# Kernel optimization log

Measured on AMD Instinct MI355X. Metric: run time of the kernel, lower is better.

The kernel has to match this reference:

```python
import jax, jax.numpy as jnp
import numpy as np

N, E = 20000, 320000
FX, FW, FH, H = 256, 128, 128, 4  # x feat, walk feat, hidden=end_embd, heads


def _gat(x, edge_index, W, a_s, a_d, R):
    # W: [H,Fin,Fout]; a_s,a_d: [H,Fout]; R: [Fin,Fout] residual projection
    n = x.shape[0]
    h = jnp.einsum('nf,hfo->hno', x, W)                      # [H,N,Fout]
    src, dst = edge_index[0], edge_index[1]
    s_src = jnp.einsum('hno,ho->nh', h, a_s)                 # [N,H]
    s_dst = jnp.einsum('hno,ho->nh', h, a_d)                 # [N,H]
    e = jax.nn.leaky_relu(s_src[src] + s_dst[dst], 0.2)      # [E,H] per-edge scores
    m = jax.ops.segment_max(e, src, num_segments=n)          # scatter-softmax (stable)
    ex = jnp.exp(e - m[src])
    den = jax.ops.segment_sum(ex, src, num_segments=n)
    alpha = ex / (den[src] + 1e-16)                          # [E,H]
    msg = jnp.transpose(h, (1, 0, 2))[dst] * alpha[:, :, None]        # [E,H,Fout]
    agg = jax.ops.segment_sum(msg, src, num_segments=n).mean(axis=1)  # [N,Fout]
    return jax.nn.elu(agg + x @ R)


def _forward(x, dat, W1, a1s, a1d, R1, W2, a2s, a2d, R2,
             Wd1, ad1s, ad1d, Rd1, Wd2, ad2s, ad2d, Rd2,
             fc1_w, fc1_b, fc2_w, fc2_b, conv_w, conv_b, edge_index):
    x1 = _gat(x, edge_index, W1, a1s, a1d, R1)
    x2 = _gat(x1, edge_index, W2, a2s, a2d, R2)
    d1 = _gat(dat, edge_index, Wd1, ad1s, ad1d, Rd1)
    d2 = _gat(d1, edge_index, Wd2, ad2s, ad2d, Rd2)
    n = x.shape[0]
    # cat on feature dim, transpose, view(1, l*2, end_size, N)
    xd = jnp.concatenate([x1, x2, d1, d2], axis=1).T.reshape(1, 4, FH, n)
    avg = xd.mean(axis=(2, 3))                               # SE global avg pool [1,4]
    att = jax.nn.sigmoid((avg @ fc1_w + fc1_b) @ fc2_w + fc2_b)  # no act between fc1/fc2 (as in source)
    xatt = jax.nn.relu(att[:, :, None, None] * xd)
    y = jnp.einsum('bchn,c->bhn', xatt, conv_w) + conv_b     # 1x1 conv, 4->1 channels
    return y.reshape(FH, n).T                                # dropout = identity (eval)


def setup_inputs():
    key = jax.random.key(0)
    ks = jax.random.split(key, 26)

    def rn(k, shape, s=0.1):
        return jax.random.normal(k, shape, jnp.float32) * s

    return {
        'x': jax.random.normal(ks[0], (N, FX), jnp.float32),
        'dat': jax.random.normal(ks[1], (N, FW), jnp.float32),
        'W1': rn(ks[2], (H, FX, FH)), 'a1s': rn(ks[3], (H, FH)), 'a1d': rn(ks[4], (H, FH)), 'R1': rn(ks[5], (FX, FH)),
        'W2': rn(ks[6], (H, FH, FH)), 'a2s': rn(ks[7], (H, FH)), 'a2d': rn(ks[8], (H, FH)), 'R2': rn(ks[9], (FH, FH)),
        'Wd1': rn(ks[10], (H, FW, FH)), 'ad1s': rn(ks[11], (H, FH)), 'ad1d': rn(ks[12], (H, FH)), 'Rd1': rn(ks[13], (FW, FH)),
        'Wd2': rn(ks[14], (H, FH, FH)), 'ad2s': rn(ks[15], (H, FH)), 'ad2d': rn(ks[16], (H, FH)), 'Rd2': rn(ks[17], (FH, FH)),
        'fc1_w': rn(ks[18], (4, 20)), 'fc1_b': jnp.zeros((20,), jnp.float32),
        'fc2_w': rn(ks[19], (20, 4)), 'fc2_b': jnp.zeros((4,), jnp.float32),
        'conv_w': rn(ks[20], (4,)), 'conv_b': jnp.zeros((), jnp.float32),
        'edge_index': jax.random.randint(ks[21], (2, E), 0, N, dtype=jnp.int32),
    }


def reference(x, dat, W1, a1s, a1d, R1, W2, a2s, a2d, R2,
              Wd1, ad1s, ad1d, Rd1, Wd2, ad2s, ad2d, Rd2,
              fc1_w, fc1_b, fc2_w, fc2_b, conv_w, conv_b, edge_index):
    return _forward(x, dat, W1, a1s, a1d, R1, W2, a2s, a2d, R2,
                    Wd1, ad1s, ad1d, Rd1, Wd2, ad2s, ad2d, Rd2,
                    fc1_w, fc1_b, fc2_w, fc2_b, conv_w, conv_b, edge_index)
```

## Files before the change

### kernel.cpp

```cpp
#include <hip/hip_runtime.h>
#include <hip/hip_bf16.h>
#include <math.h>

#define NN 20000
#define EE 320000
#define FXX 256
#define FWW 128
#define NH 4

typedef __attribute__((ext_vector_type(8))) short short8v;
typedef __attribute__((ext_vector_type(4))) float f32x4;

static __device__ __forceinline__ float bf2f(unsigned short s) {
    unsigned int u = ((unsigned int)s) << 16;
    return __builtin_bit_cast(float, u);
}

static __device__ __forceinline__ unsigned short f2bf_u16(float f) {
    unsigned int u = __builtin_bit_cast(unsigned int, f);
    unsigned int r = 0x7fffu + ((u >> 16) & 1u);
    return (unsigned short)((u + r) >> 16);
}

struct WscItem { const float* W; const float* as_; const float* ad_; int Fin; };
struct WscParams { WscItem t[4]; };

__global__ __launch_bounds__(256) void wsc_kernel(WscParams p, float* __restrict__ wsc)
{
    int L = blockIdx.z;
    WscItem it = p.t[L];
    int wid = threadIdx.x >> 6, lane = threadIdx.x & 63;
    int r = blockIdx.x * 4 + wid;
    if (r >= it.Fin * 4) return;
    int h = r / it.Fin, k = r - h * it.Fin;
    float2 w2 = *(const float2*)(it.W + ((size_t)(h * it.Fin + k)) * 128 + 2 * lane);
    float2 s2 = *(const float2*)(it.as_ + h * 128 + 2 * lane);
    float2 d2 = *(const float2*)(it.ad_ + h * 128 + 2 * lane);
    float vs = w2.x * s2.x + w2.y * s2.y;
    float vd = w2.x * d2.x + w2.y * d2.y;
    #pragma unroll
    for (int o = 32; o; o >>= 1) { vs += __shfl_xor(vs, o); vd += __shfl_xor(vd, o); }
    if (lane == 0) {
        wsc[(size_t)L * 2048 + h * 256 + k] = vs;
        wsc[(size_t)L * 2048 + (4 + h) * 256 + k] = vd;
    }
}

struct WcItem { const float* W; const float* R; __hip_bfloat16* dst; int Fin; int KK; int total; };
struct WcParams { WcItem t[4]; };

__global__ __launch_bounds__(256) void wcomb_kernel(WcParams p)
{
    WcItem it = p.t[blockIdx.z];
    int idx = blockIdx.x * 256 + threadIdx.x;
    if (idx >= it.total) return;
    int c = idx / it.KK;
    int k5 = idx - c * it.KK;
    int f4 = it.Fin * 4;
    float v;
    if (k5 < f4) {
        int h = k5 / it.Fin, k = k5 - h * it.Fin;
        v = 0.25f * it.W[((size_t)(h * it.Fin + k)) * 128 + c];
    } else {
        v = it.R[(size_t)(k5 - f4) * 128 + c];
    }
    it.dst[(size_t)c * it.KK + k5] = __float2bfloat16(v);
}

template<int CF>
static __device__ __forceinline__ void cast_score_body(const float* __restrict__ Xf,
                                                       __hip_bfloat16* __restrict__ Xb,
                                                       const float* __restrict__ wsc,
                                                       float* __restrict__ ssrc,
                                                       float* __restrict__ sdst)
{
    const int Fin = CF * 64;
    int wid = threadIdx.x >> 6, lane = threadIdx.x & 63;
    int n = blockIdx.x * 4 + wid;
    if (n >= NN) return;
    int c0 = lane * CF;
    float xv[CF];
    #pragma unroll
    for (int i = 0; i < CF; ++i) xv[i] = Xf[(size_t)n * Fin + c0 + i];
    union { unsigned u[CF / 2]; unsigned short s[CF]; } pk;
    #pragma unroll
    for (int i = 0; i < CF; ++i) pk.s[i] = f2bf_u16(xv[i]);
    #pragma unroll
    for (int w = 0; w < CF / 2; ++w)
        *(unsigned*)(Xb + (size_t)n * Fin + c0 + w * 2) = pk.u[w];
    float acc[8];
    #pragma unroll
    for (int j = 0; j < 8; ++j) {
        const float* w = wsc + j * 256 + c0;
        float s = 0.f;
        #pragma unroll
        for (int i = 0; i < CF; ++i) s += xv[i] * w[i];
        acc[j] = s;
    }
    #pragma unroll
    for (int o = 32; o; o >>= 1)
        #pragma unroll
        for (int j = 0; j < 8; ++j) acc[j] += __shfl_xor(acc[j], o);
    if (lane == 0) {
        *(float4*)(ssrc + (size_t)n * 4) = make_float4(acc[0], acc[1], acc[2], acc[3]);
        *(float4*)(sdst + (size_t)n * 4) = make_float4(acc[4], acc[5], acc[6], acc[7]);
    }
}

struct CSPair {
    const float* Xf[2]; __hip_bfloat16* Xb[2];
    const float* wsc[2]; float* ssrc[2]; float* sdst[2];
};

__global__ __launch_bounds__(256) void cast_score_pair(CSPair p)
{
    if (blockIdx.y == 0)
        cast_score_body<4>(p.Xf[0], p.Xb[0], p.wsc[0], p.ssrc[0], p.sdst[0]);
    else
        cast_score_body<2>(p.Xf[1], p.Xb[1], p.wsc[1], p.ssrc[1], p.sdst[1]);
}

__global__ __launch_bounds__(256) void hist_kernel(const int* __restrict__ src, int* __restrict__ cnt)
{
    int i = blockIdx.x * blockDim.x + threadIdx.x;
    if (i < EE) atomicAdd(&cnt[src[i]], 1);
}

__global__ __launch_bounds__(1024) void scan_kernel(const int* __restrict__ cnt, int* __restrict__ row_ptr)
{
    __shared__ int lds[1024];
    int t = threadIdx.x;
    const int CH = 20;
    int start = t * CH, end = start + CH; if (end > NN) end = NN;
    int sum = 0;
    if (start < NN) for (int i = start; i < end; ++i) sum += cnt[i];
    lds[t] = sum;
    __syncthreads();
    for (int o = 1; o < 1024; o <<= 1) {
        int v = (t >= o) ? lds[t - o] : 0;
        __syncthreads();
        lds[t] += v;
        __syncthreads();
    }
    int run = lds[t] - sum;
    if (start < NN) for (int i = start; i < end; ++i) { row_ptr[i] = run; run += cnt[i]; }
    if (t == 1023) row_ptr[NN] = lds[1023];
}

__global__ __launch_bounds__(256) void scatter_kernel(const int* __restrict__ src,
                                                      const int* __restrict__ dst,
                                                      const int* __restrict__ row_ptr,
                                                      int* __restrict__ off,
                                                      int* __restrict__ csr_dst)
{
    int i = blockIdx.x * blockDim.x + threadIdx.x;
    if (i >= EE) return;
    int s = src[i];
    int p = row_ptr[s] + atomicAdd(&off[s], 1);
    csr_dst[p] = dst[i];
}

template<int CF>
static __device__ __forceinline__ void agg_body(const __hip_bfloat16* __restrict__ Xb,
                                                const float* __restrict__ ssrc,
                                                const float* __restrict__ sdst,
                                                const int* __restrict__ row_ptr,
                                                const int* __restrict__ csr_dst,
                                                __hip_bfloat16* __restrict__ Cat)
{
    const int Fin = CF * 64, F4 = 4 * Fin;
    int wid = threadIdx.x >> 6, lane = threadIdx.x & 63;
    int n = blockIdx.x * 4 + wid;
    if (n >= NN) return;
    int r0 = row_ptr[n], r1 = row_ptr[n + 1];
    int deg = r1 - r0;

    float acc[4][CF] = {};

    if (deg > 0) {
        float4 sn = *(const float4*)(ssrc + (size_t)n * 4);
        auto comp_e = [&](int s, int& dout) -> float4 {
            int d = csr_dst[r0 + s];
            dout = d;
            float4 sd = *(const float4*)(sdst + (size_t)d * 4);
            float4 e; float v;
            v = sn.x + sd.x; e.x = v >= 0.f ? v : 0.2f * v;
            v = sn.y + sd.y; e.y = v >= 0.f ? v : 0.2f * v;
            v = sn.z + sd.z; e.z = v >= 0.f ? v : 0.2f * v;
            v = sn.w + sd.w; e.w = v >= 0.f ? v : 0.2f * v;
            return e;
        };

        float4 e0 = make_float4(-1e30f, -1e30f, -1e30f, -1e30f);
        int d0 = 0;
        if (lane < deg) e0 = comp_e(lane, d0);
        float4 m = e0;
        for (int s = lane + 64; s < deg; s += 64) {
            int dt; float4 ev = comp_e(s, dt);
            m.x = fmaxf(m.x, ev.x); m.y = fmaxf(m.y, ev.y);
            m.z = fmaxf(m.z, ev.z); m.w = fmaxf(m.w, ev.w);
        }
        #pragma unroll
        for (int o = 32; o; o >>= 1) {
            m.x = fmaxf(m.x, __shfl_xor(m.x, o));
            m.y = fmaxf(m.y, __shfl_xor(m.y, o));
            m.z = fmaxf(m.z, __shfl_xor(m.z, o));
            m.w = fmaxf(m.w, __shfl_xor(m.w, o));
        }
        float4 p0 = make_float4(0.f, 0.f, 0.f, 0.f);
        if (lane < deg) {
            p0.x = expf(e0.x - m.x); p0.y = expf(e0.y - m.y);
            p0.z = expf(e0.z - m.z); p0.w = expf(e0.w - m.w);
        }
        float4 den = p0;
        for (int s = lane + 64; s < deg; s += 64) {
            int dt; float4 ev = comp_e(s, dt);
            den.x += expf(ev.x - m.x); den.y += expf(ev.y - m.y);
            den.z += expf(ev.z - m.z); den.w += expf(ev.w - m.w);
        }
        #pragma unroll
        for (int o = 32; o; o >>= 1) {
            den.x += __shfl_xor(den.x, o); den.y += __shfl_xor(den.y, o);
            den.z += __shfl_xor(den.z, o); den.w += __shfl_xor(den.w, o);
        }
        den.x = 1.f / (den.x + 1e-16f); den.y = 1.f / (den.y + 1e-16f);
        den.z = 1.f / (den.z + 1e-16f); den.w = 1.f / (den.w + 1e-16f);

        float4 a0;
        a0.x = p0.x * den.x; a0.y = p0.y * den.y;
        a0.z = p0.z * den.z; a0.w = p0.w * den.w;

        int cnt0 = min(deg, 64);
        int last = cnt0 - 1;
        for (int base = 0; base < cnt0; base += 4) {
            int j1 = min(base + 1, last), j2 = min(base + 2, last), j3 = min(base + 3, last);
            int dv0 = __shfl(d0, base), dv1 = __shfl(d0, j1);
            int dv2 = __shfl(d0, j2),   dv3 = __shfl(d0, j3);
            union U { unsigned u[CF / 2]; unsigned short s[CF]; };
            U l0, l1, l2, l3;
            #pragma unroll
            for (int w = 0; w < CF / 2; ++w)
                l0.u[w] = *(const unsigned*)(Xb + (size_t)dv0 * Fin + lane * CF + w * 2);
            #pragma unroll
            for (int w = 0; w < CF / 2; ++w)
                l1.u[w] = *(const unsigned*)(Xb + (size_t)dv1 * Fin + lane * CF + w * 2);
            #pragma unroll
            for (int w = 0; w < CF / 2; ++w)
                l2.u[w] = *(const unsigned*)(Xb + (size_t)dv2 * Fin + lane * CF + w * 2);
            #pragma unroll
            for (int w = 0; w < CF / 2; ++w)
                l3.u[w] = *(const unsigned*)(Xb + (size_t)dv3 * Fin + lane * CF + w * 2);

            {
                float ax = __shfl(a0.x, base), ay = __shfl(a0.y, base);
                float az = __shfl(a0.z, base), aw = __shfl(a0.w, base);
                #pragma unroll
                for (int i = 0; i < CF; ++i) {
                    float xv = bf2f(l0.s[i]);
                    acc[0][i] += ax * xv; acc[1][i] += ay * xv;
                    acc[2][i] += az * xv; acc[3][i] += aw * xv;
                }
            }
            if (base + 1 < cnt0) {
                float ax = __shfl(a0.x, j1), ay = __shfl(a0.y, j1);
                float az = __shfl(a0.z, j1), aw = __shfl(a0.w, j1);
                #pragma unroll
                for (int i = 0; i < CF; ++i) {
                    float xv = bf2f(l1.s[i]);
                    acc[0][i] += ax * xv; acc[1][i] += ay * xv;
                    acc[2][i] += az * xv; acc[3][i] += aw * xv;
                }
            }
            if (base + 2 < cnt0) {
                float ax = __shfl(a0.x, j2), ay = __shfl(a0.y, j2);
                float az = __shfl(a0.z, j2), aw = __shfl(a0.w, j2);
                #pragma unroll
                for (int i = 0; i < CF; ++i) {
                    float xv = bf2f(l2.s[i]);
                    acc[0][i] += ax * xv; acc[1][i] += ay * xv;
                    acc[2][i] += az * xv; acc[3][i] += aw * xv;
                }
            }
            if (base + 3 < cnt0) {
                float ax = __shfl(a0.x, j3), ay = __shfl(a0.y, j3);
                float az = __shfl(a0.z, j3), aw = __shfl(a0.w, j3);
                #pragma unroll
                for (int i = 0; i < CF; ++i) {
                    float xv = bf2f(l3.s[i]);
                    acc[0][i] += ax * xv; acc[1][i] += ay * xv;
                    acc[2][i] += az * xv; acc[3][i] += aw * xv;
                }
            }
        }

        for (int r = r0 + 64; r < r1; r += 64) {
            int cnt = min(64, r1 - r);
            int d = 0;
            float4 a4 = make_float4(0.f, 0.f, 0.f, 0.f);
            if (r + lane < r1) {
                int dt;
                float4 ev = comp_e(r - r0 + lane, dt);
                d = dt;
                a4.x = expf(ev.x - m.x) * den.x; a4.y = expf(ev.y - m.y) * den.y;
                a4.z = expf(ev.z - m.z) * den.z; a4.w = expf(ev.w - m.w) * den.w;
            }
            for (int j = 0; j < cnt; ++j) {
                int ddv = __shfl(d, j);
                float ax = __shfl(a4.x, j), ay = __shfl(a4.y, j);
                float az = __shfl(a4.z, j), aw = __shfl(a4.w, j);
                union { unsigned u[CF / 2]; unsigned short s[CF]; } ld;
                #pragma unroll
                for (int w = 0; w < CF / 2; ++w)
                    ld.u[w] = *(const unsigned*)(Xb + (size_t)ddv * Fin + lane * CF + w * 2);
                #pragma unroll
                for (int i = 0; i < CF; ++i) {
                    float xv = bf2f(ld.s[i]);
                    acc[0][i] += ax * xv; acc[1][i] += ay * xv;
                    acc[2][i] += az * xv; acc[3][i] += aw * xv;
                }
            }
        }
    }

    __hip_bfloat16* crow = Cat + (size_t)n * F4;
    #pragma unroll
    for (int h = 0; h < 4; ++h) {
        union { unsigned u[CF / 2]; unsigned short s[CF]; } pk;
        #pragma unroll
        for (int i = 0; i < CF; ++i) pk.s[i] = f2bf_u16(acc[h][i]);
        #pragma unroll
        for (int w = 0; w < CF / 2; ++w)
            *(unsigned*)(crow + h * Fin + lane * CF + w * 2) = pk.u[w];
    }
}

struct AggPair {
    const __hip_bfloat16* Xb[2];
    const float* ssrc[2]; const float* sdst[2];
    __hip_bfloat16* Cat[2];
};

template<int CF0, int CF1>
__global__ __launch_bounds__(256) void agg_pair_kernel(AggPair p,
                                                       const int* __restrict__ row_ptr,
                                                       const int* __restrict__ csr_dst)
{
    if (blockIdx.y == 0)
        agg_body<CF0>(p.Xb[0], p.ssrc[0], p.sdst[0], row_ptr, csr_dst, p.Cat[0]);
    else
        agg_body<CF1>(p.Xb[1], p.ssrc[1], p.sdst[1], row_ptr, csr_dst, p.Cat[1]);
}

struct GemmArgs {
    const __hip_bfloat16 *Cat, *Xb, *Wct;
    float* xout; __hip_bfloat16* xbout;
    const float* wscN; float *ssrcN, *sdstN;
    int F4, FIN, ch;
};
struct GemmPair { GemmArgs g[2]; };

__global__ __launch_bounds__(256) void gemm_pair_kernel(GemmPair p, float* __restrict__ sums)
{
    GemmArgs a = (blockIdx.y == 0) ? p.g[0] : p.g[1];
    const int F4 = a.F4, FIN = a.FIN;
    const int KK = F4 + FIN;
    const int BK = 64;
    const int NIT = KK / BK;
    __shared__ short As[2][32 * 72];
    __shared__ short Bs[2][128 * 72];
    __shared__ float ls[4];
    __shared__ float sred[4][4][4][8];

    int tid = threadIdx.x, lane = tid & 63, wid = tid >> 6;
    int wr = wid >> 1, wc = wid & 1;
    int ar = lane & 15, kg = lane >> 4;
    int row0 = blockIdx.x * 32;

    int a_row = tid >> 3, a_seg = tid & 7;
    int b_col = tid >> 1, b_seg0 = (tid & 1) * 4;

    const __hip_bfloat16* AgC = a.Cat + (size_t)(row0 + a_row) * F4 + a_seg * 8;
    const __hip_bfloat16* AgX = a.Xb + (size_t)(row0 + a_row) * FIN + a_seg * 8;
    const __hip_bfloat16* Bg = a.Wct + (size_t)b_col * KK + b_seg0 * 8;

    short8v fa, fb0, fb1, fb2, fb3;
    f32x4 acc[4] = {};

    fa  = *(const short8v*)(AgC);
    fb0 = *(const short8v*)(Bg);
    fb1 = *(const short8v*)(Bg + 8);
    fb2 = *(const short8v*)(Bg + 16);
    fb3 = *(const short8v*)(Bg + 24);
    *(short8v*)(&As[0][a_row * 72 + a_seg * 8]) = fa;
    *(short8v*)(&Bs[0][b_col * 72 + (b_seg0 + 0) * 8]) = fb0;
    *(short8v*)(&Bs[0][b_col * 72 + (b_seg0 + 1) * 8]) = fb1;
    *(short8v*)(&Bs[0][b_col * 72 + (b_seg0 + 2) * 8]) = fb2;
    *(short8v*)(&Bs[0][b_col * 72 + (b_seg0 + 3) * 8]) = fb3;

    int cur = 0;
    for (int it = 0; it < NIT; ++it) {
        if (it + 1 < NIT) {
            int kb = (it + 1) * BK;
            fa  = (kb < F4) ? *(const short8v*)(AgC + kb) : *(const short8v*)(AgX + (kb - F4));
            fb0 = *(const short8v*)(Bg + kb);
            fb1 = *(const short8v*)(Bg + kb + 8);
            fb2 = *(const short8v*)(Bg + kb + 16);
            fb3 = *(const short8v*)(Bg + kb + 24);
        }
        __syncthreads();
        #pragma unroll
        for (int ks = 0; ks < 2; ++ks) {
            short8v av = *(const short8v*)(&As[cur][(wr * 16 + ar) * 72 + ks * 32 + kg * 8]);
            #pragma unroll
            for (int nb = 0; nb < 4; ++nb) {
                short8v bv = *(const short8v*)(&Bs[cur][(wc * 64 + nb * 16 + ar) * 72 + ks * 32 + kg * 8]);
                acc[nb] = __builtin_amdgcn_mfma_f32_16x16x32_bf16(av, bv, acc[nb], 0, 0, 0);
            }
        }
        if (it + 1 < NIT) {
            int nb2 = cur ^ 1;
            *(short8v*)(&As[nb2][a_row * 72 + a_seg * 8]) = fa;
            *(short8v*)(&Bs[nb2][b_col * 72 + (b_seg0 + 0) * 8]) = fb0;
            *(short8v*)(&Bs[nb2][b_col * 72 + (b_seg0 + 1) * 8]) = fb1;
            *(short8v*)(&Bs[nb2][b_col * 72 + (b_seg0 + 2) * 8]) = fb2;
            *(short8v*)(&Bs[nb2][b_col * 72 + (b_seg0 + 3) * 8]) = fb3;
        }
        cur ^= 1;
    }

    float lsum = 0.f;
    float vpost[4][4];
    int rsub = (lane >> 4) * 4;
    #pragma unroll
    for (int nb = 0; nb < 4; ++nb) {
        int col = wc * 64 + nb * 16 + ar;
        #pragma unroll
        for (int r = 0; r < 4; ++r) {
            int row = row0 + wr * 16 + rsub + r;
            float v = acc[nb][r];
            v = v > 0.f ? v : expm1f(v);
            vpost[nb][r] = v;
            lsum += v;
            a.xout[(size_t)row * 128 + col] = v;
            a.xbout[(size_t)row * 128 + col] = __float2bfloat16(v);
        }
    }
    #pragma unroll
    for (int o = 32; o; o >>= 1) lsum += __shfl_xor(lsum, o);
    if (lane == 0) ls[wid] = lsum;

    bool dosc = a.wscN != nullptr;
    if (dosc) {
        float sc[4][8] = {};
        #pragma unroll
        for (int j = 0; j < 8; ++j) {
            #pragma unroll
            for (int nb = 0; nb < 4; ++nb) {
                float wv = a.wscN[j * 256 + wc * 64 + nb * 16 + ar];
                #pragma unroll
                for (int r = 0; r < 4; ++r) sc[r][j] += vpost[nb][r] * wv;
            }
        }
        #pragma unroll
        for (int o = 8; o; o >>= 1)
            #pragma unroll
            for (int r = 0; r < 4; ++r)
                #pragma unroll
                for (int j = 0; j < 8; ++j) sc[r][j] += __shfl_xor(sc[r][j], o);
        if (ar == 0) {
            int grp = lane >> 4;
            #pragma unroll
            for (int r = 0; r < 4; ++r)
                #pragma unroll
                for (int j = 0; j < 8; ++j) sred[wid][grp][r][j] = sc[r][j];
        }
    }
    __syncthreads();
    if (tid == 0) atomicAdd(&sums[a.ch], ls[0] + ls[1] + ls[2] + ls[3]);
    if (dosc) {
        int row_local = tid >> 3, j = tid & 7;
        int w_r = row_local >> 4, grp = (row_local >> 2) & 3, r = row_local & 3;
        float total = sred[w_r * 2 + 0][grp][r][j] + sred[w_r * 2 + 1][grp][r][j];
        int row = row0 + row_local;
        if (j < 4) a.ssrcN[(size_t)row * 4 + j] = total;
        else       a.sdstN[(size_t)row * 4 + (j - 4)] = total;
    }
}

__global__ void att_kernel(const float* __restrict__ sums,
                           const float* __restrict__ fc1w, const float* __restrict__ fc1b,
                           const float* __restrict__ fc2w, const float* __restrict__ fc2b,
                           float* __restrict__ att)
{
    if (threadIdx.x != 0 || blockIdx.x != 0) return;
    float avg[4];
    for (int c = 0; c < 4; ++c) avg[c] = sums[c] * (1.f / (NN * 128.f));
    float z[20];
    for (int j = 0; j < 20; ++j) {
        float v = fc1b[j];
        for (int c = 0; c < 4; ++c) v += avg[c] * fc1w[c * 20 + j];
        z[j] = v;
    }
    for (int c = 0; c < 4; ++c) {
        float v = fc2b[c];
        for (int j = 0; j < 20; ++j) v += z[j] * fc2w[j * 4 + c];
        att[c] = 1.f / (1.f + expf(-v));
    }
}

__global__ __launch_bounds__(256) void final_kernel(const float* __restrict__ x1,
                                                    const float* __restrict__ x2,
                                                    const float* __restrict__ d1,
                                                    const float* __restrict__ d2,
                                                    const float* __restrict__ att,
                                                    const float* __restrict__ convw,
                                                    const float* __restrict__ convb,
                                                    float* __restrict__ out)
{
    int i = blockIdx.x * blockDim.x + threadIdx.x;
    if (i >= NN * 128) return;
    float a0 = att[0], a1 = att[1], a2 = att[2], a3 = att[3];
    float w0 = convw[0], w1 = convw[1], w2 = convw[2], w3 = convw[3];
    float v = convb[0];
    v += w0 * fmaxf(a0 * x1[i], 0.f);
    v += w1 * fmaxf(a1 * x2[i], 0.f);
    v += w2 * fmaxf(a2 * d1[i], 0.f);
    v += w3 * fmaxf(a3 * d2[i], 0.f);
    out[i] = v;
}

extern "C" void kernel_launch(void* const* d_in, const int* in_sizes, int n_in,
                              void* d_out, int out_size, void* d_ws, size_t ws_size,
                              hipStream_t stream)
{
    (void)in_sizes; (void)n_in; (void)out_size; (void)ws_size;
    const float* x    = (const float*)d_in[0];
    const float* dat  = (const float*)d_in[1];
    const float* W1   = (const float*)d_in[2];
    const float* a1s  = (const float*)d_in[3];
    const float* a1d  = (const float*)d_in[4];
    const float* R1   = (const float*)d_in[5];
    const float* W2   = (const float*)d_in[6];
    const float* a2s  = (const float*)d_in[7];
    const float* a2d  = (const float*)d_in[8];
    const float* R2   = (const float*)d_in[9];
    const float* Wd1  = (const float*)d_in[10];
    const float* ad1s = (const float*)d_in[11];
    const float* ad1d = (const float*)d_in[12];
    const float* Rd1  = (const float*)d_in[13];
    const float* Wd2  = (const float*)d_in[14];
    const float* ad2s = (const float*)d_in[15];
    const float* ad2d = (const float*)d_in[16];
    const float* Rd2  = (const float*)d_in[17];
    const float* fc1w = (const float*)d_in[18];
    const float* fc1b = (const float*)d_in[19];
    const float* fc2w = (const float*)d_in[20];
    const float* fc2b = (const float*)d_in[21];
    const float* convw= (const float*)d_in[22];
    const float* convb= (const float*)d_in[23];
    const int*   eidx = (const int*)d_in[24];
    const int* esrc = eidx;
    const int* edst = eidx + EE;
    float* out = (float*)d_out;

    char* base = (char*)d_ws;
    size_t woff = 0;
    auto alloc = [&](size_t bytes) -> void* {
        void* p = base + woff;
        woff = (woff + bytes + 255) & ~(size_t)255;
        return p;
    };
    __hip_bfloat16* Cat0 = (__hip_bfloat16*)alloc((size_t)NN * 1024 * 2);
    __hip_bfloat16* Cat2 = (__hip_bfloat16*)alloc((size_t)NN * 512 * 2);
    float* X1    = (float*)alloc((size_t)NN * 128 * 4);
    float* X2    = (float*)alloc((size_t)NN * 128 * 4);
    float* D1    = (float*)alloc((size_t)NN * 128 * 4);
    float* D2    = (float*)alloc((size_t)NN * 128 * 4);
    __hip_bfloat16* XbX   = (__hip_bfloat16*)alloc((size_t)NN * FXX * 2);
    __hip_bfloat16* XbDat = (__hip_bfloat16*)alloc((size_t)NN * FWW * 2);
    __hip_bfloat16* Xb1   = (__hip_bfloat16*)alloc((size_t)NN * 128 * 2);
    __hip_bfloat16* XbD1  = (__hip_bfloat16*)alloc((size_t)NN * 128 * 2);
    __hip_bfloat16* XbTmp = (__hip_bfloat16*)alloc((size_t)NN * 128 * 2);
    __hip_bfloat16* XbTm2 = (__hip_bfloat16*)alloc((size_t)NN * 128 * 2);
    float* Wsc   = (float*)alloc((size_t)4 * 2048 * 4);
    __hip_bfloat16* Wct0 = (__hip_bfloat16*)alloc((size_t)128 * 1280 * 2);
    __hip_bfloat16* Wct1 = (__hip_bfloat16*)alloc((size_t)128 * 640 * 2);
    __hip_bfloat16* Wct2 = (__hip_bfloat16*)alloc((size_t)128 * 640 * 2);
    __hip_bfloat16* Wct3 = (__hip_bfloat16*)alloc((size_t)128 * 640 * 2);
    float* SsrcX = (float*)alloc((size_t)NN * 4 * 4);
    float* SdstX = (float*)alloc((size_t)NN * 4 * 4);
    float* Ssrc1 = (float*)alloc((size_t)NN * 4 * 4);
    float* Sdst1 = (float*)alloc((size_t)NN * 4 * 4);
    float* SsrcD = (float*)alloc((size_t)NN * 4 * 4);
    float* SdstD = (float*)alloc((size_t)NN * 4 * 4);
    float* Ssrc3 = (float*)alloc((size_t)NN * 4 * 4);
    float* Sdst3 = (float*)alloc((size_t)NN * 4 * 4);
    int* RowPtr  = (int*)alloc((size_t)(NN + 1) * 4);
    int* Cnt     = (int*)alloc((size_t)NN * 4);
    int* Off     = (int*)alloc((size_t)NN * 4);
    int* CsrDst  = (int*)alloc((size_t)EE * 4);
    float* Sums  = (float*)alloc(16);
    float* Att   = (float*)alloc(16);

    {
        WscParams WP;
        WP.t[0] = { W1,  a1s,  a1d,  FXX };
        WP.t[1] = { W2,  a2s,  a2d,  FWW };
        WP.t[2] = { Wd1, ad1s, ad1d, FWW };
        WP.t[3] = { Wd2, ad2s, ad2d, FWW };
        wsc_kernel<<<dim3(256, 1, 4), 256, 0, stream>>>(WP, Wsc);
        WcParams CP;
        CP.t[0] = { W1,  R1,  Wct0, FXX, 1280, 128 * 1280 };
        CP.t[1] = { W2,  R2,  Wct1, FWW, 640,  128 * 640 };
        CP.t[2] = { Wd1, Rd1, Wct2, FWW, 640,  128 * 640 };
        CP.t[3] = { Wd2, Rd2, Wct3, FWW, 640,  128 * 640 };
        wcomb_kernel<<<dim3(640, 1, 4), 256, 0, stream>>>(CP);
        CSPair CS;
        CS.Xf[0] = x;   CS.Xb[0] = XbX;   CS.wsc[0] = Wsc;            CS.ssrc[0] = SsrcX; CS.sdst[0] = SdstX;
        CS.Xf[1] = dat; CS.Xb[1] = XbDat; CS.wsc[1] = Wsc + 2 * 2048; CS.ssrc[1] = SsrcD; CS.sdst[1] = SdstD;
        cast_score_pair<<<dim3((NN + 3) / 4, 2), 256, 0, stream>>>(CS);
    }
    hipMemsetAsync(Cnt, 0, (size_t)NN * 4, stream);
    hipMemsetAsync(Off, 0, (size_t)NN * 4, stream);
    hipMemsetAsync(Sums, 0, 16, stream);
    hist_kernel<<<(EE + 255) / 256, 256, 0, stream>>>(esrc, Cnt);
    scan_kernel<<<1, 1024, 0, stream>>>(Cnt, RowPtr);
    scatter_kernel<<<(EE + 255) / 256, 256, 0, stream>>>(esrc, edst, RowPtr, Off, CsrDst);

    {
        AggPair AP;
        AP.Xb[0] = XbX;   AP.ssrc[0] = SsrcX; AP.sdst[0] = SdstX; AP.Cat[0] = Cat0;
        AP.Xb[1] = XbDat; AP.ssrc[1] = SsrcD; AP.sdst[1] = SdstD; AP.Cat[1] = Cat2;
        agg_pair_kernel<4, 2><<<dim3((NN + 3) / 4, 2), 256, 0, stream>>>(AP, RowPtr, CsrDst);
    }
    {
        GemmPair GP;
        GP.g[0] = { Cat0, XbX,   Wct0, X1, Xb1,  Wsc + 1 * 2048, Ssrc1, Sdst1, 1024, 256, 0 };
        GP.g[1] = { Cat2, XbDat, Wct2, D1, XbD1, Wsc + 3 * 2048, Ssrc3, Sdst3, 512,  128, 2 };
        gemm_pair_kernel<<<dim3(NN / 32, 2), 256, 0, stream>>>(GP, Sums);
    }
    {
        AggPair AP;
        AP.Xb[0] = Xb1;  AP.ssrc[0] = Ssrc1; AP.sdst[0] = Sdst1; AP.Cat[0] = Cat0;
        AP.Xb[1] = XbD1; AP.ssrc[1] = Ssrc3; AP.sdst[1] = Sdst3; AP.Cat[1] = Cat2;
        agg_pair_kernel<2, 2><<<dim3((NN + 3) / 4, 2), 256, 0, stream>>>(AP, RowPtr, CsrDst);
    }
    {
        GemmPair GP;
        GP.g[0] = { Cat0, Xb1,  Wct1, X2, XbTmp, nullptr, nullptr, nullptr, 512, 128, 1 };
        GP.g[1] = { Cat2, XbD1, Wct3, D2, XbTm2, nullptr, nullptr, nullptr, 512, 128, 3 };
        gemm_pair_kernel<<<dim3(NN / 32, 2), 256, 0, stream>>>(GP, Sums);
    }

    att_kernel<<<1, 64, 0, stream>>>(Sums, fc1w, fc1b, fc2w, fc2b, Att);
    final_kernel<<<(NN * 128 + 255) / 256, 256, 0, stream>>>(X1, X2, D1, D2, Att, convw, convb, out);
}
```

Before: 307.4 us.

## Drop fp32 layer outputs, fuse SE attention into bf16 final kernel

The GEMM epilogue no longer writes fp32 copies of each layer output, and only bf16 outputs are kept. The final combine kernel reads the four bf16 tensors two elements at a time and recomputes the small SE attention MLP per thread, which removes the separate single-thread att kernel launch. This cuts global write and read traffic roughly in half for those tensors. In exchange the final output is computed from bf16-rounded activations, and every thread repeats the tiny MLP.

```diff
diff --git a/kernel.cpp b/kernel.cpp
--- a/kernel.cpp
+++ b/kernel.cpp
@@ -353,7 +353,7 @@
 
 struct GemmArgs {
     const __hip_bfloat16 *Cat, *Xb, *Wct;
-    float* xout; __hip_bfloat16* xbout;
+    __hip_bfloat16* xbout;
     const float* wscN; float *ssrcN, *sdstN;
     int F4, FIN, ch;
 };
@@ -441,7 +441,6 @@
             v = v > 0.f ? v : expm1f(v);
             vpost[nb][r] = v;
             lsum += v;
-            a.xout[(size_t)row * 128 + col] = v;
             a.xbout[(size_t)row * 128 + col] = __float2bfloat16(v);
         }
     }
@@ -487,46 +486,56 @@
     }
 }
 
-__global__ void att_kernel(const float* __restrict__ sums,
-                           const float* __restrict__ fc1w, const float* __restrict__ fc1b,
-                           const float* __restrict__ fc2w, const float* __restrict__ fc2b,
-                           float* __restrict__ att)
-{
-    if (threadIdx.x != 0 || blockIdx.x != 0) return;
-    float avg[4];
-    for (int c = 0; c < 4; ++c) avg[c] = sums[c] * (1.f / (NN * 128.f));
-    float z[20];
-    for (int j = 0; j < 20; ++j) {
-        float v = fc1b[j];
-        for (int c = 0; c < 4; ++c) v += avg[c] * fc1w[c * 20 + j];
-        z[j] = v;
-    }
-    for (int c = 0; c < 4; ++c) {
-        float v = fc2b[c];
-        for (int j = 0; j < 20; ++j) v += z[j] * fc2w[j * 4 + c];
-        att[c] = 1.f / (1.f + expf(-v));
-    }
-}
-
-__global__ __launch_bounds__(256) void final_kernel(const float* __restrict__ x1,
-                                                    const float* __restrict__ x2,
-                                                    const float* __restrict__ d1,
-                                                    const float* __restrict__ d2,
-                                                    const float* __restrict__ att,
+__global__ __launch_bounds__(256) void final_kernel(const __hip_bfloat16* __restrict__ x1,
+                                                    const __hip_bfloat16* __restrict__ x2,
+                                                    const __hip_bfloat16* __restrict__ d1,
+                                                    const __hip_bfloat16* __restrict__ d2,
+                                                    const float* __restrict__ sums,
+                                                    const float* __restrict__ fc1w, const float* __restrict__ fc1b,
+                                                    const float* __restrict__ fc2w, const float* __restrict__ fc2b,
                                                     const float* __restrict__ convw,
                                                     const float* __restrict__ convb,
                                                     float* __restrict__ out)
 {
-    int i = blockIdx.x * blockDim.x + threadIdx.x;
+    float att[4];
+    {
+        float avg[4];
+        #pragma unroll
+        for (int c = 0; c < 4; ++c) avg[c] = sums[c] * (1.f / (NN * 128.f));
+        float z[20];
+        #pragma unroll
+        for (int j = 0; j < 20; ++j) {
+            float v = fc1b[j];
+            #pragma unroll
+            for (int c = 0; c < 4; ++c) v += avg[c] * fc1w[c * 20 + j];
+            z[j] = v;
+        }
+        #pragma unroll
+        for (int c = 0; c < 4; ++c) {
+            float v = fc2b[c];
+            #pragma unroll
+            for (int j = 0; j < 20; ++j) v += z[j] * fc2w[j * 4 + c];
+            att[c] = 1.f / (1.f + expf(-v));
+        }
+    }
+    int i = (blockIdx.x * 256 + threadIdx.x) * 2;
     if (i >= NN * 128) return;
-    float a0 = att[0], a1 = att[1], a2 = att[2], a3 = att[3];
+    unsigned u1 = *(const unsigned*)(x1 + i);
+    unsigned u2 = *(const unsigned*)(x2 + i);
+    unsigned u3 = *(const unsigned*)(d1 + i);
+    unsigned u4 = *(const unsigned*)(d2 + i);
     float w0 = convw[0], w1 = convw[1], w2 = convw[2], w3 = convw[3];
-    float v = convb[0];
-    v += w0 * fmaxf(a0 * x1[i], 0.f);
-    v += w1 * fmaxf(a1 * x2[i], 0.f);
-    v += w2 * fmaxf(a2 * d1[i], 0.f);
-    v += w3 * fmaxf(a3 * d2[i], 0.f);
-    out[i] = v;
+    float cb = convb[0];
+    float2 r;
+    r.x = cb + w0 * fmaxf(att[0] * bf2f((unsigned short)(u1 & 0xffff)), 0.f)
+             + w1 * fmaxf(att[1] * bf2f((unsigned short)(u2 & 0xffff)), 0.f)
+             + w2 * fmaxf(att[2] * bf2f((unsigned short)(u3 & 0xffff)), 0.f)
+             + w3 * fmaxf(att[3] * bf2f((unsigned short)(u4 & 0xffff)), 0.f);
+    r.y = cb + w0 * fmaxf(att[0] * bf2f((unsigned short)(u1 >> 16)), 0.f)
+             + w1 * fmaxf(att[1] * bf2f((unsigned short)(u2 >> 16)), 0.f)
+             + w2 * fmaxf(att[2] * bf2f((unsigned short)(u3 >> 16)), 0.f)
+             + w3 * fmaxf(att[3] * bf2f((unsigned short)(u4 >> 16)), 0.f);
+    *(float2*)(out + i) = r;
 }
 
 extern "C" void kernel_launch(void* const* d_in, const int* in_sizes, int n_in,
@@ -572,16 +581,12 @@
     };
     __hip_bfloat16* Cat0 = (__hip_bfloat16*)alloc((size_t)NN * 1024 * 2);
     __hip_bfloat16* Cat2 = (__hip_bfloat16*)alloc((size_t)NN * 512 * 2);
-    float* X1    = (float*)alloc((size_t)NN * 128 * 4);
-    float* X2    = (float*)alloc((size_t)NN * 128 * 4);
-    float* D1    = (float*)alloc((size_t)NN * 128 * 4);
-    float* D2    = (float*)alloc((size_t)NN * 128 * 4);
     __hip_bfloat16* XbX   = (__hip_bfloat16*)alloc((size_t)NN * FXX * 2);
     __hip_bfloat16* XbDat = (__hip_bfloat16*)alloc((size_t)NN * FWW * 2);
     __hip_bfloat16* Xb1   = (__hip_bfloat16*)alloc((size_t)NN * 128 * 2);
     __hip_bfloat16* XbD1  = (__hip_bfloat16*)alloc((size_t)NN * 128 * 2);
-    __hip_bfloat16* XbTmp = (__hip_bfloat16*)alloc((size_t)NN * 128 * 2);
-    __hip_bfloat16* XbTm2 = (__hip_bfloat16*)alloc((size_t)NN * 128 * 2);
+    __hip_bfloat16* Xb2   = (__hip_bfloat16*)alloc((size_t)NN * 128 * 2);
+    __hip_bfloat16* XbD2  = (__hip_bfloat16*)alloc((size_t)NN * 128 * 2);
     float* Wsc   = (float*)alloc((size_t)4 * 2048 * 4);
     __hip_bfloat16* Wct0 = (__hip_bfloat16*)alloc((size_t)128 * 1280 * 2);
     __hip_bfloat16* Wct1 = (__hip_bfloat16*)alloc((size_t)128 * 640 * 2);
@@ -600,7 +605,6 @@
     int* Off     = (int*)alloc((size_t)NN * 4);
     int* CsrDst  = (int*)alloc((size_t)EE * 4);
     float* Sums  = (float*)alloc(16);
-    float* Att   = (float*)alloc(16);
 
     {
         WscParams WP;
@@ -635,8 +639,8 @@
     }
     {
         GemmPair GP;
-        GP.g[0] = { Cat0, XbX,   Wct0, X1, Xb1,  Wsc + 1 * 2048, Ssrc1, Sdst1, 1024, 256, 0 };
-        GP.g[1] = { Cat2, XbDat, Wct2, D1, XbD1, Wsc + 3 * 2048, Ssrc3, Sdst3, 512,  128, 2 };
+        GP.g[0] = { Cat0, XbX,   Wct0, Xb1,  Wsc + 1 * 2048, Ssrc1, Sdst1, 1024, 256, 0 };
+        GP.g[1] = { Cat2, XbDat, Wct2, XbD1, Wsc + 3 * 2048, Ssrc3, Sdst3, 512,  128, 2 };
         gemm_pair_kernel<<<dim3(NN / 32, 2), 256, 0, stream>>>(GP, Sums);
     }
     {
@@ -647,11 +651,12 @@
     }
     {
         GemmPair GP;
-        GP.g[0] = { Cat0, Xb1,  Wct1, X2, XbTmp, nullptr, nullptr, nullptr, 512, 128, 1 };
-        GP.g[1] = { Cat2, XbD1, Wct3, D2, XbTm2, nullptr, nullptr, nullptr, 512, 128, 3 };
+        GP.g[0] = { Cat0, Xb1,  Wct1, Xb2,  nullptr, nullptr, nullptr, 512, 128, 1 };
+        GP.g[1] = { Cat2, XbD1, Wct3, XbD2, nullptr, nullptr, nullptr, 512, 128, 3 };
         gemm_pair_kernel<<<dim3(NN / 32, 2), 256, 0, stream>>>(GP, Sums);
     }
 
-    att_kernel<<<1, 64, 0, stream>>>(Sums, fc1w, fc1b, fc2w, fc2b, Att);
-    final_kernel<<<(NN * 128 + 255) / 256, 256, 0, stream>>>(X1, X2, D1, D2, Att, convw, convb, out);
-}
+    final_kernel<<<(NN * 128 / 2 + 255) / 256, 256, 0, stream>>>(Xb1, Xb2, XbD1, XbD2, Sums,
+                                                                 fc1w, fc1b, fc2w, fc2b,
+                                                                 convw, convb, out);
+}
```

After: 322.3 us. 1.05x slower.
